# Optimization experiments

Hardware: AMD Instinct MI355X
Metric: run time of the kernel (lower is better)

Reference implementation:

```python
import jax, jax.numpy as jnp
import numpy as np

D_MODEL = 1024
NUM_HEADS = 16
D_K = D_MODEL // NUM_HEADS
CLAMP = 1e9
EPS = 1e-12


def setup_inputs() -> dict:
    key = jax.random.key(0)
    ks = jax.random.split(key, 11)
    B, S, D = 4, 2048, D_MODEL
    std = 1.0 / np.sqrt(D)
    inp = {
        'Q': jax.random.normal(ks[0], (B, S, D), jnp.float32),
        'K': jax.random.normal(ks[1], (B, S, D), jnp.float32),
        'V': jax.random.normal(ks[2], (B, S, D), jnp.float32),
        'Wq': jax.random.normal(ks[3], (D, D), jnp.float32) * std,
        'bq': jnp.zeros((D,), jnp.float32),
        'Wk': jax.random.normal(ks[4], (D, D), jnp.float32) * std,
        'bk': jnp.zeros((D,), jnp.float32),
        'Wv': jax.random.normal(ks[5], (D, D), jnp.float32) * std,
        'bv': jnp.zeros((D,), jnp.float32),
        'Wo': jax.random.normal(ks[6], (D, D), jnp.float32) * std,
        'bo': jnp.zeros((D,), jnp.float32),
    }
    return inp


def _split_heads(x):
    b, s, _ = x.shape
    return x.reshape(b, s, NUM_HEADS, D_K).transpose(0, 2, 1, 3)  # [b,h,s,dk]


def reference(Q, K, V, Wq, bq, Wk, bk, Wv, bv, Wo, bo):
    Qh = _split_heads(Q @ Wq.T + bq)
    Kh = _split_heads(K @ Wk.T + bk)
    Vh = _split_heads(V @ Wv.T + bv)
    scale = jnp.sqrt(jnp.asarray(D_K, Qh.dtype))
    scores = jnp.einsum('bhqd,bhkd->bhqk', Qh, Kh) / scale
    scores = scores - jnp.max(scores, axis=-1, keepdims=True)
    scores = jnp.clip(scores, -CLAMP, CLAMP)
    attn = jax.nn.softmax(scores, axis=-1)
    attn = jnp.clip(attn, EPS, None)
    attn = attn / jnp.sum(attn, axis=-1, keepdims=True)
    ctx = jnp.einsum('bhqk,bhkd->bhqd', attn, Vh)
    b, h, s, dk = ctx.shape
    ctx = ctx.transpose(0, 2, 1, 3).reshape(b, s, D_MODEL)
    return ctx @ Wo.T + bo
```

## Files before the change

### kernel.cpp

```cpp
#include <hip/hip_runtime.h>
#include <hip/hip_bf16.h>


typedef float  f32x4  __attribute__((ext_vector_type(4)));
typedef __bf16 bf16x8 __attribute__((ext_vector_type(8)));
typedef short  s16x8  __attribute__((ext_vector_type(8)));

#define MFMA16(a,b,c) __builtin_amdgcn_mfma_f32_16x16x32_bf16((a),(b),(c),0,0,0)

__device__ __forceinline__ unsigned short f2bf(float f) {
    union { float f; unsigned u; } v; v.f = f;
    unsigned r = v.u + 0x7fffu + ((v.u >> 16) & 1u);
    return (unsigned short)(r >> 16);
}

__device__ __forceinline__ s16x8 cvt8(const float* __restrict__ p) {
    f32x4 x = *(const f32x4*)p;
    f32x4 y = *(const f32x4*)(p + 4);
    s16x8 r;
    r[0] = (short)f2bf(x[0]); r[1] = (short)f2bf(x[1]);
    r[2] = (short)f2bf(x[2]); r[3] = (short)f2bf(x[3]);
    r[4] = (short)f2bf(y[0]); r[5] = (short)f2bf(y[1]);
    r[6] = (short)f2bf(y[2]); r[7] = (short)f2bf(y[3]);
    return r;
}

__device__ __forceinline__ void gl_lds16(const void* g, void* l) {
    __builtin_amdgcn_global_load_lds(
        (const __attribute__((address_space(1))) unsigned int*)g,
        (__attribute__((address_space(3))) unsigned int*)l, 16, 0, 0);
}

__global__ __launch_bounds__(256) void cvt_kernel(
    const float* __restrict__ src, unsigned short* __restrict__ dst, int n8)
{
    int i = blockIdx.x * 256 + threadIdx.x;
    if (i < n8) *(s16x8*)(dst + (size_t)i * 8) = cvt8(src + (size_t)i * 8);
}

template <int MODE>
__global__ __launch_bounds__(256) void gemm_bf16(
    const unsigned short* __restrict__ A,
    const unsigned short* __restrict__ W,
    const float* __restrict__ bias,
    void* __restrict__ Cv)
{
    constexpr int K = 1024;
    __shared__ unsigned short Ash[128 * 32];
    __shared__ unsigned short Bsh[128 * 32];

    const int t    = threadIdx.x;
    const int w    = t >> 6;
    const int lane = t & 63;
    const int wm   = w >> 1, wn = w & 1;
    const int lr   = lane & 15, quad = lane >> 4;

    const int m0 = blockIdx.y * 128;
    const int n0 = blockIdx.x * 128;

    const int srow = t >> 2;
    const int skp  = (t & 3) * 8;

    const unsigned short* Ap0 = A + (size_t)(m0 + srow) * K + skp;
    const unsigned short* Ap1 = Ap0 + (size_t)64 * K;
    const unsigned short* Wp0 = W + (size_t)(n0 + srow) * K + skp;
    const unsigned short* Wp1 = Wp0 + (size_t)64 * K;
    unsigned short* lA0 = &Ash[w * 512];
    unsigned short* lA1 = &Ash[2048 + w * 512];
    unsigned short* lB0 = &Bsh[w * 512];
    unsigned short* lB1 = &Bsh[2048 + w * 512];

    f32x4 acc[4][4] = {};

    for (int k0 = 0; k0 < K; k0 += 32) {
        __syncthreads();
        gl_lds16(Ap0 + k0, lA0);
        gl_lds16(Ap1 + k0, lA1);
        gl_lds16(Wp0 + k0, lB0);
        gl_lds16(Wp1 + k0, lB1);
        __syncthreads();

        bf16x8 af[4], bw[4];
#pragma unroll
        for (int i = 0; i < 4; i++)
            af[i] = *(const bf16x8*)&Ash[(wm * 64 + i * 16 + lr) * 32 + quad * 8];
#pragma unroll
        for (int j = 0; j < 4; j++)
            bw[j] = *(const bf16x8*)&Bsh[(wn * 64 + j * 16 + lr) * 32 + quad * 8];

#pragma unroll
        for (int i = 0; i < 4; i++)
#pragma unroll
            for (int j = 0; j < 4; j++)
                acc[i][j] = MFMA16(af[i], bw[j], acc[i][j]);
    }

#pragma unroll
    for (int i = 0; i < 4; i++) {
#pragma unroll
        for (int j = 0; j < 4; j++) {
            const int n = n0 + wn * 64 + j * 16 + lr;
#pragma unroll
            for (int r = 0; r < 4; r++) {
                const int m = m0 + wm * 64 + i * 16 + quad * 4 + r;
                float val = acc[i][j][r] + ((MODE == 2) ? bias[m] : bias[n]);
                if (MODE == 0) {
                    const int b = m >> 11, s = m & 2047, h = n >> 6, d = n & 63;
                    ((unsigned short*)Cv)[(((size_t)(b * 16 + h) * 2048 + s) << 6) + d] = f2bf(val);
                } else if (MODE == 1) {
                    ((float*)Cv)[(size_t)m * 1024 + n] = val;
                } else {
                    const int h = m >> 6, d = m & 63, b = n >> 11, s = n & 2047;
                    ((unsigned short*)Cv)[((size_t)(b * 16 + h) * 64 + d) * 2048 + s] = f2bf(val);
                }
            }
        }
    }
}

__global__ __launch_bounds__(256) void attn_kernel(
    const unsigned short* __restrict__ Qh,
    const unsigned short* __restrict__ Kh,
    const unsigned short* __restrict__ Vt,
    unsigned short* __restrict__ ctx)
{
    constexpr int KS = 72;
    __shared__ unsigned short Ksh[64 * KS];
    __shared__ unsigned short Vts[64 * KS];
    __shared__ unsigned short Psh[4][16 * KS];

    const int t    = threadIdx.x;
    const int w    = t >> 6;
    const int lane = t & 63;
    const int lr   = lane & 15, quad = lane >> 4;

    const int bh = blockIdx.y, qblk = blockIdx.x;
    const size_t base = (size_t)bh * 2048 * 64;
    const unsigned short* Qp = Qh + base;
    const unsigned short* Kg = Kh + base + (size_t)lane * 64 + w * 16;
    const unsigned short* Vg = Vt + base + (size_t)lane * 2048 + w * 16;

    const int q0 = qblk * 64 + w * 16;
    bf16x8 aq0 = *(const bf16x8*)(Qp + (size_t)(q0 + lr) * 64 + quad * 8);
    bf16x8 aq1 = *(const bf16x8*)(Qp + (size_t)(q0 + lr) * 64 + 32 + quad * 8);

    f32x4 Of[4] = {};
    float lsum[4] = {0.f, 0.f, 0.f, 0.f};

    for (int kb = 0; kb < 2048; kb += 64) {
        s16x8 kv0 = *(const s16x8*)(Kg + (size_t)kb * 64);
        s16x8 kv1 = *(const s16x8*)(Kg + (size_t)kb * 64 + 8);
        s16x8 vv0 = *(const s16x8*)(Vg + kb);
        s16x8 vv1 = *(const s16x8*)(Vg + kb + 8);

        __syncthreads();
        *(s16x8*)&Ksh[lane * KS + w * 16]     = kv0;
        *(s16x8*)&Ksh[lane * KS + w * 16 + 8] = kv1;
        *(s16x8*)&Vts[lane * KS + w * 16]     = vv0;
        *(s16x8*)&Vts[lane * KS + w * 16 + 8] = vv1;
        __syncthreads();

        f32x4 sc[4];
#pragma unroll
        for (int nt = 0; nt < 4; nt++) {
            const unsigned short* kr = &Ksh[(16 * nt + lr) * KS + quad * 8];
            f32x4 c = {};
            c = MFMA16(aq0, *(const bf16x8*)kr, c);
            c = MFMA16(aq1, *(const bf16x8*)(kr + 32), c);
            sc[nt] = c;
        }

#pragma unroll
        for (int r = 0; r < 4; r++) {
            float p0 = __expf(sc[0][r] * 0.125f);
            float p1 = __expf(sc[1][r] * 0.125f);
            float p2 = __expf(sc[2][r] * 0.125f);
            float p3 = __expf(sc[3][r] * 0.125f);
            lsum[r] += (p0 + p1) + (p2 + p3);
            unsigned short* pr = &Psh[w][(quad * 4 + r) * KS + lr];
            pr[0]  = f2bf(p0);
            pr[16] = f2bf(p1);
            pr[32] = f2bf(p2);
            pr[48] = f2bf(p3);
        }
        __asm__ __volatile__("s_waitcnt lgkmcnt(0)" ::: "memory");

        bf16x8 pf0 = *(const bf16x8*)&Psh[w][lr * KS + quad * 8];
        bf16x8 pf1 = *(const bf16x8*)&Psh[w][lr * KS + 32 + quad * 8];
#pragma unroll
        for (int dt = 0; dt < 4; dt++) {
            const unsigned short* vr = &Vts[(dt * 16 + lr) * KS + quad * 8];
            Of[dt] = MFMA16(pf0, *(const bf16x8*)vr, Of[dt]);
            Of[dt] = MFMA16(pf1, *(const bf16x8*)(vr + 32), Of[dt]);
        }
    }

    const int b = bh >> 4, h = bh & 15;
#pragma unroll
    for (int r = 0; r < 4; r++) {
        float l = lsum[r];
        l += __shfl_xor(l, 1);
        l += __shfl_xor(l, 2);
        l += __shfl_xor(l, 4);
        l += __shfl_xor(l, 8);
        const float inv = 1.0f / l;
        const int q = q0 + quad * 4 + r;
        unsigned short* cp = ctx + ((size_t)b * 2048 + q) * 1024 + h * 64;
#pragma unroll
        for (int dt = 0; dt < 4; dt++)
            cp[dt * 16 + lr] = f2bf(Of[dt][r] * inv);
    }
}

extern "C" void kernel_launch(void* const* d_in, const int* in_sizes, int n_in,
                              void* d_out, int out_size, void* d_ws, size_t ws_size,
                              hipStream_t stream) {
    const float* Q  = (const float*)d_in[0];
    const float* K  = (const float*)d_in[1];
    const float* V  = (const float*)d_in[2];
    const float* Wq = (const float*)d_in[3];
    const float* bq = (const float*)d_in[4];
    const float* Wk = (const float*)d_in[5];
    const float* bk = (const float*)d_in[6];
    const float* Wv = (const float*)d_in[7];
    const float* bv = (const float*)d_in[8];
    const float* Wo = (const float*)d_in[9];
    const float* bo = (const float*)d_in[10];

    const size_t EB = (size_t)8192 * 1024;
    const size_t EW = (size_t)1024 * 1024;
    unsigned short* Xb  = (unsigned short*)d_ws;
    unsigned short* Wqb = Xb  + EB;
    unsigned short* Wkb = Wqb + EW;
    unsigned short* Wvb = Wkb + EW;
    unsigned short* Wob = Wvb + EW;
    unsigned short* Qh  = Wob + EW;
    unsigned short* Kh  = Qh  + EB;
    unsigned short* Vtw = Kh  + EB;
    unsigned short* Ctx = Xb;

    const int n8b = (int)(EB / 8);
    const int n8w = (int)(EW / 8);

    cvt_kernel<<<n8w / 256, 256, 0, stream>>>(Wq, Wqb, n8w);
    cvt_kernel<<<n8w / 256, 256, 0, stream>>>(Wk, Wkb, n8w);
    cvt_kernel<<<n8w / 256, 256, 0, stream>>>(Wv, Wvb, n8w);
    cvt_kernel<<<n8w / 256, 256, 0, stream>>>(Wo, Wob, n8w);

    dim3 tb(256), gP(8, 64), gT(64, 8);

    cvt_kernel<<<n8b / 256, 256, 0, stream>>>(Q, Xb, n8b);
    gemm_bf16<0><<<gP, tb, 0, stream>>>(Xb, Wqb, bq, Qh);

    cvt_kernel<<<n8b / 256, 256, 0, stream>>>(K, Xb, n8b);
    gemm_bf16<0><<<gP, tb, 0, stream>>>(Xb, Wkb, bk, Kh);

    cvt_kernel<<<n8b / 256, 256, 0, stream>>>(V, Xb, n8b);
    gemm_bf16<2><<<gT, tb, 0, stream>>>(Wvb, Xb, bv, Vtw);

    attn_kernel<<<dim3(32, 64), tb, 0, stream>>>(Qh, Kh, Vtw, Ctx);

    gemm_bf16<1><<<gP, tb, 0, stream>>>(Ctx, Wob, bo, (float*)d_out);
}
```

Measured before the change: 424.7 us.

## Batch QKV projections into one launch, vectorize epilogues, widen attention query tiles

The three input projections now run as a single launch that picks its operands from blockIdx.z, when the workspace is large enough to hold separate bf16 copies of Q, K and V. The GEMM operands are swapped so each lane stores four contiguous outputs, which turns scalar epilogue stores into vector stores. The attention kernel gives each wave 64 query rows instead of 16, so every K/V tile staged in LDS is reused four times more, at the cost of more registers, a larger P buffer and a quarter as many blocks. Lower occupancy and fewer blocks could hurt latency hiding.

```diff
diff --git a/kernel.cpp b/kernel.cpp
--- a/kernel.cpp
+++ b/kernel.cpp
@@ -5,6 +5,7 @@
 typedef float  f32x4  __attribute__((ext_vector_type(4)));
 typedef __bf16 bf16x8 __attribute__((ext_vector_type(8)));
 typedef short  s16x8  __attribute__((ext_vector_type(8)));
+typedef short  s16x4  __attribute__((ext_vector_type(4)));
 
 #define MFMA16(a,b,c) __builtin_amdgcn_mfma_f32_16x16x32_bf16((a),(b),(c),0,0,0)
 
@@ -38,33 +39,44 @@
     if (i < n8) *(s16x8*)(dst + (size_t)i * 8) = cvt8(src + (size_t)i * 8);
 }
 
-template <int MODE>
-__global__ __launch_bounds__(256) void gemm_bf16(
-    const unsigned short* __restrict__ A,
-    const unsigned short* __restrict__ W,
-    const float* __restrict__ bias,
-    void* __restrict__ Cv)
+__global__ __launch_bounds__(256) void gemm_fused(
+    const unsigned short* __restrict__ A0, const unsigned short* __restrict__ B0,
+    const float* __restrict__ c0, void* __restrict__ d0, int m0_,
+    const unsigned short* __restrict__ A1, const unsigned short* __restrict__ B1,
+    const float* __restrict__ c1, void* __restrict__ d1, int m1_,
+    const unsigned short* __restrict__ A2, const unsigned short* __restrict__ B2,
+    const float* __restrict__ c2, void* __restrict__ d2, int m2_,
+    int zforce)
 {
+    const int z = (zforce >= 0) ? zforce : (int)blockIdx.z;
+    const unsigned short* A = (z == 0) ? A0 : (z == 1) ? A1 : A2;
+    const unsigned short* B = (z == 0) ? B0 : (z == 1) ? B1 : B2;
+    const float* bias       = (z == 0) ? c0 : (z == 1) ? c1 : c2;
+    void* dst               = (z == 0) ? d0 : (z == 1) ? d1 : d2;
+    const int mode          = (z == 0) ? m0_ : (z == 1) ? m1_ : m2_;
+
     constexpr int K = 1024;
     __shared__ unsigned short Ash[128 * 32];
     __shared__ unsigned short Bsh[128 * 32];
 
     const int t    = threadIdx.x;
     const int w    = t >> 6;
+    const int wm   = w >> 1, wn = w & 1;
     const int lane = t & 63;
-    const int wm   = w >> 1, wn = w & 1;
     const int lr   = lane & 15, quad = lane >> 4;
 
-    const int m0 = blockIdx.y * 128;
-    const int n0 = blockIdx.x * 128;
+    const int ta = (mode == 2) ? (int)blockIdx.x : (int)blockIdx.y;
+    const int tb = (mode == 2) ? (int)blockIdx.y : (int)blockIdx.x;
+    const int a0 = ta * 128;
+    const int b0 = tb * 128;
 
     const int srow = t >> 2;
     const int skp  = (t & 3) * 8;
 
-    const unsigned short* Ap0 = A + (size_t)(m0 + srow) * K + skp;
+    const unsigned short* Ap0 = A + (size_t)(a0 + srow) * K + skp;
     const unsigned short* Ap1 = Ap0 + (size_t)64 * K;
-    const unsigned short* Wp0 = W + (size_t)(n0 + srow) * K + skp;
-    const unsigned short* Wp1 = Wp0 + (size_t)64 * K;
+    const unsigned short* Bp0 = B + (size_t)(b0 + srow) * K + skp;
+    const unsigned short* Bp1 = Bp0 + (size_t)64 * K;
     unsigned short* lA0 = &Ash[w * 512];
     unsigned short* lA1 = &Ash[2048 + w * 512];
     unsigned short* lB0 = &Bsh[w * 512];
@@ -76,8 +88,8 @@
         __syncthreads();
         gl_lds16(Ap0 + k0, lA0);
         gl_lds16(Ap1 + k0, lA1);
-        gl_lds16(Wp0 + k0, lB0);
-        gl_lds16(Wp1 + k0, lB1);
+        gl_lds16(Bp0 + k0, lB0);
+        gl_lds16(Bp1 + k0, lB1);
         __syncthreads();
 
         bf16x8 af[4], bw[4];
@@ -99,20 +111,30 @@
     for (int i = 0; i < 4; i++) {
 #pragma unroll
         for (int j = 0; j < 4; j++) {
-            const int n = n0 + wn * 64 + j * 16 + lr;
-#pragma unroll
-            for (int r = 0; r < 4; r++) {
-                const int m = m0 + wm * 64 + i * 16 + quad * 4 + r;
-                float val = acc[i][j][r] + ((MODE == 2) ? bias[m] : bias[n]);
-                if (MODE == 0) {
-                    const int b = m >> 11, s = m & 2047, h = n >> 6, d = n & 63;
-                    ((unsigned short*)Cv)[(((size_t)(b * 16 + h) * 2048 + s) << 6) + d] = f2bf(val);
-                } else if (MODE == 1) {
-                    ((float*)Cv)[(size_t)m * 1024 + n] = val;
-                } else {
-                    const int h = m >> 6, d = m & 63, b = n >> 11, s = n & 2047;
-                    ((unsigned short*)Cv)[((size_t)(b * 16 + h) * 64 + d) * 2048 + s] = f2bf(val);
-                }
+            const int fa = a0 + wm * 64 + i * 16 + quad * 4;
+            const int cb = b0 + wn * 64 + j * 16 + lr;
+            if (mode == 0) {
+                f32x4 bb = *(const f32x4*)(bias + fa);
+                const int h = fa >> 6, d = fa & 63;
+                const int bb_ = cb >> 11, s = cb & 2047;
+                s16x4 pk;
+#pragma unroll
+                for (int r = 0; r < 4; r++) pk[r] = (short)f2bf(acc[i][j][r] + bb[r]);
+                *(s16x4*)((unsigned short*)dst +
+                          (((size_t)(bb_ * 16 + h) * 2048 + s) << 6) + d) = pk;
+            } else if (mode == 1) {
+                f32x4 bb = *(const f32x4*)(bias + fa);
+                f32x4 v  = acc[i][j] + bb;
+                *(f32x4*)((float*)dst + (size_t)cb * 1024 + fa) = v;
+            } else {
+                const float bb = bias[cb];
+                const int h = cb >> 6, d = cb & 63;
+                const int bb_ = fa >> 11, s = fa & 2047;
+                s16x4 pk;
+#pragma unroll
+                for (int r = 0; r < 4; r++) pk[r] = (short)f2bf(acc[i][j][r] + bb);
+                *(s16x4*)((unsigned short*)dst +
+                          ((size_t)(bb_ * 16 + h) * 64 + d) * 2048 + s) = pk;
             }
         }
     }
@@ -127,7 +149,7 @@
     constexpr int KS = 72;
     __shared__ unsigned short Ksh[64 * KS];
     __shared__ unsigned short Vts[64 * KS];
-    __shared__ unsigned short Psh[4][16 * KS];
+    __shared__ unsigned short Psh[4][64 * KS];
 
     const int t    = threadIdx.x;
     const int w    = t >> 6;
@@ -140,12 +162,18 @@
     const unsigned short* Kg = Kh + base + (size_t)lane * 64 + w * 16;
     const unsigned short* Vg = Vt + base + (size_t)lane * 2048 + w * 16;
 
-    const int q0 = qblk * 64 + w * 16;
-    bf16x8 aq0 = *(const bf16x8*)(Qp + (size_t)(q0 + lr) * 64 + quad * 8);
-    bf16x8 aq1 = *(const bf16x8*)(Qp + (size_t)(q0 + lr) * 64 + 32 + quad * 8);
-
-    f32x4 Of[4] = {};
-    float lsum[4] = {0.f, 0.f, 0.f, 0.f};
+    const int q0 = qblk * 256 + w * 64;
+
+    bf16x8 aq0[4], aq1[4];
+#pragma unroll
+    for (int s4 = 0; s4 < 4; s4++) {
+        const unsigned short* qp = Qp + (size_t)(q0 + s4 * 16 + lr) * 64 + quad * 8;
+        aq0[s4] = *(const bf16x8*)qp;
+        aq1[s4] = *(const bf16x8*)(qp + 32);
+    }
+
+    f32x4 Of[4][4] = {};
+    float lsum[4][4] = {};
 
     for (int kb = 0; kb < 2048; kb += 64) {
         s16x8 kv0 = *(const s16x8*)(Kg + (size_t)kb * 64);
@@ -160,55 +188,76 @@
         *(s16x8*)&Vts[lane * KS + w * 16 + 8] = vv1;
         __syncthreads();
 
-        f32x4 sc[4];
+        bf16x8 bk0[4], bk1[4];
 #pragma unroll
         for (int nt = 0; nt < 4; nt++) {
             const unsigned short* kr = &Ksh[(16 * nt + lr) * KS + quad * 8];
-            f32x4 c = {};
-            c = MFMA16(aq0, *(const bf16x8*)kr, c);
-            c = MFMA16(aq1, *(const bf16x8*)(kr + 32), c);
-            sc[nt] = c;
-        }
-
-#pragma unroll
-        for (int r = 0; r < 4; r++) {
-            float p0 = __expf(sc[0][r] * 0.125f);
-            float p1 = __expf(sc[1][r] * 0.125f);
-            float p2 = __expf(sc[2][r] * 0.125f);
-            float p3 = __expf(sc[3][r] * 0.125f);
-            lsum[r] += (p0 + p1) + (p2 + p3);
-            unsigned short* pr = &Psh[w][(quad * 4 + r) * KS + lr];
-            pr[0]  = f2bf(p0);
-            pr[16] = f2bf(p1);
-            pr[32] = f2bf(p2);
-            pr[48] = f2bf(p3);
+            bk0[nt] = *(const bf16x8*)kr;
+            bk1[nt] = *(const bf16x8*)(kr + 32);
+        }
+#pragma unroll
+        for (int sub = 0; sub < 4; sub++) {
+            f32x4 sc[4];
+#pragma unroll
+            for (int nt = 0; nt < 4; nt++) {
+                f32x4 c = {};
+                c = MFMA16(aq0[sub], bk0[nt], c);
+                c = MFMA16(aq1[sub], bk1[nt], c);
+                sc[nt] = c;
+            }
+#pragma unroll
+            for (int r = 0; r < 4; r++) {
+                float p0 = __expf(sc[0][r] * 0.125f);
+                float p1 = __expf(sc[1][r] * 0.125f);
+                float p2 = __expf(sc[2][r] * 0.125f);
+                float p3 = __expf(sc[3][r] * 0.125f);
+                lsum[sub][r] += (p0 + p1) + (p2 + p3);
+                unsigned short* pr = &Psh[w][(sub * 16 + quad * 4 + r) * KS + lr];
+                pr[0]  = f2bf(p0);
+                pr[16] = f2bf(p1);
+                pr[32] = f2bf(p2);
+                pr[48] = f2bf(p3);
+            }
         }
         __asm__ __volatile__("s_waitcnt lgkmcnt(0)" ::: "memory");
 
-        bf16x8 pf0 = *(const bf16x8*)&Psh[w][lr * KS + quad * 8];
-        bf16x8 pf1 = *(const bf16x8*)&Psh[w][lr * KS + 32 + quad * 8];
+        bf16x8 bv0[4], bv1[4];
 #pragma unroll
         for (int dt = 0; dt < 4; dt++) {
             const unsigned short* vr = &Vts[(dt * 16 + lr) * KS + quad * 8];
-            Of[dt] = MFMA16(pf0, *(const bf16x8*)vr, Of[dt]);
-            Of[dt] = MFMA16(pf1, *(const bf16x8*)(vr + 32), Of[dt]);
+            bv0[dt] = *(const bf16x8*)vr;
+            bv1[dt] = *(const bf16x8*)(vr + 32);
+        }
+#pragma unroll
+        for (int sub = 0; sub < 4; sub++) {
+            const unsigned short* pp = &Psh[w][(sub * 16 + lr) * KS + quad * 8];
+            bf16x8 pf0 = *(const bf16x8*)pp;
+            bf16x8 pf1 = *(const bf16x8*)(pp + 32);
+#pragma unroll
+            for (int dt = 0; dt < 4; dt++) {
+                Of[sub][dt] = MFMA16(pf0, bv0[dt], Of[sub][dt]);
+                Of[sub][dt] = MFMA16(pf1, bv1[dt], Of[sub][dt]);
+            }
         }
     }
 
     const int b = bh >> 4, h = bh & 15;
 #pragma unroll
-    for (int r = 0; r < 4; r++) {
-        float l = lsum[r];
-        l += __shfl_xor(l, 1);
-        l += __shfl_xor(l, 2);
-        l += __shfl_xor(l, 4);
-        l += __shfl_xor(l, 8);
-        const float inv = 1.0f / l;
-        const int q = q0 + quad * 4 + r;
-        unsigned short* cp = ctx + ((size_t)b * 2048 + q) * 1024 + h * 64;
-#pragma unroll
-        for (int dt = 0; dt < 4; dt++)
-            cp[dt * 16 + lr] = f2bf(Of[dt][r] * inv);
+    for (int sub = 0; sub < 4; sub++) {
+#pragma unroll
+        for (int r = 0; r < 4; r++) {
+            float l = lsum[sub][r];
+            l += __shfl_xor(l, 1);
+            l += __shfl_xor(l, 2);
+            l += __shfl_xor(l, 4);
+            l += __shfl_xor(l, 8);
+            const float inv = 1.0f / l;
+            const int q = q0 + sub * 16 + quad * 4 + r;
+            unsigned short* cp = ctx + ((size_t)b * 2048 + q) * 1024 + h * 64;
+#pragma unroll
+            for (int dt = 0; dt < 4; dt++)
+                cp[dt * 16 + lr] = f2bf(Of[sub][dt][r] * inv);
+        }
     }
 }
 
@@ -229,36 +278,76 @@
 
     const size_t EB = (size_t)8192 * 1024;
     const size_t EW = (size_t)1024 * 1024;
-    unsigned short* Xb  = (unsigned short*)d_ws;
-    unsigned short* Wqb = Xb  + EB;
-    unsigned short* Wkb = Wqb + EW;
-    unsigned short* Wvb = Wkb + EW;
-    unsigned short* Wob = Wvb + EW;
-    unsigned short* Qh  = Wob + EW;
-    unsigned short* Kh  = Qh  + EB;
-    unsigned short* Vtw = Kh  + EB;
-    unsigned short* Ctx = Xb;
-
-    const int n8b = (int)(EB / 8);
-    const int n8w = (int)(EW / 8);
-
-    cvt_kernel<<<n8w / 256, 256, 0, stream>>>(Wq, Wqb, n8w);
-    cvt_kernel<<<n8w / 256, 256, 0, stream>>>(Wk, Wkb, n8w);
-    cvt_kernel<<<n8w / 256, 256, 0, stream>>>(Wv, Wvb, n8w);
-    cvt_kernel<<<n8w / 256, 256, 0, stream>>>(Wo, Wob, n8w);
-
-    dim3 tb(256), gP(8, 64), gT(64, 8);
-
-    cvt_kernel<<<n8b / 256, 256, 0, stream>>>(Q, Xb, n8b);
-    gemm_bf16<0><<<gP, tb, 0, stream>>>(Xb, Wqb, bq, Qh);
-
-    cvt_kernel<<<n8b / 256, 256, 0, stream>>>(K, Xb, n8b);
-    gemm_bf16<0><<<gP, tb, 0, stream>>>(Xb, Wkb, bk, Kh);
-
-    cvt_kernel<<<n8b / 256, 256, 0, stream>>>(V, Xb, n8b);
-    gemm_bf16<2><<<gT, tb, 0, stream>>>(Wvb, Xb, bv, Vtw);
-
-    attn_kernel<<<dim3(32, 64), tb, 0, stream>>>(Qh, Kh, Vtw, Ctx);
-
-    gemm_bf16<1><<<gP, tb, 0, stream>>>(Ctx, Wob, bo, (float*)d_out);
-}
+    const int n8b = (int)(EB / 8), n8w = (int)(EW / 8);
+    dim3 tb(256);
+
+    const bool fused = ws_size >= (6 * EB + 4 * EW) * 2;
+
+    if (fused) {
+        unsigned short* Xq  = (unsigned short*)d_ws;
+        unsigned short* Xk  = Xq + EB;
+        unsigned short* Xv  = Xk + EB;
+        unsigned short* Wqb = Xv + EB;
+        unsigned short* Wkb = Wqb + EW;
+        unsigned short* Wvb = Wkb + EW;
+        unsigned short* Wob = Wvb + EW;
+        unsigned short* Qh  = Wob + EW;
+        unsigned short* Kh  = Qh + EB;
+        unsigned short* Vtw = Kh + EB;
+        unsigned short* Ctx = Xq;
+
+        cvt_kernel<<<n8w / 256, tb, 0, stream>>>(Wq, Wqb, n8w);
+        cvt_kernel<<<n8w / 256, tb, 0, stream>>>(Wk, Wkb, n8w);
+        cvt_kernel<<<n8w / 256, tb, 0, stream>>>(Wv, Wvb, n8w);
+        cvt_kernel<<<n8w / 256, tb, 0, stream>>>(Wo, Wob, n8w);
+        cvt_kernel<<<n8b / 256, tb, 0, stream>>>(Q, Xq, n8b);
+        cvt_kernel<<<n8b / 256, tb, 0, stream>>>(K, Xk, n8b);
+        cvt_kernel<<<n8b / 256, tb, 0, stream>>>(V, Xv, n8b);
+
+        gemm_fused<<<dim3(64, 8, 3), tb, 0, stream>>>(
+            Wqb, Xq, bq, Qh, 0,
+            Wkb, Xk, bk, Kh, 0,
+            Xv, Wvb, bv, Vtw, 2,
+            -1);
+
+        attn_kernel<<<dim3(8, 64), tb, 0, stream>>>(Qh, Kh, Vtw, Ctx);
+
+        gemm_fused<<<dim3(64, 8, 1), tb, 0, stream>>>(
+            Wob, Ctx, bo, d_out, 1,
+            Wob, Ctx, bo, d_out, 1,
+            Wob, Ctx, bo, d_out, 1,
+            0);
+    } else {
+        unsigned short* Xb  = (unsigned short*)d_ws;
+        unsigned short* Wqb = Xb + EB;
+        unsigned short* Wkb = Wqb + EW;
+        unsigned short* Wvb = Wkb + EW;
+        unsigned short* Wob = Wvb + EW;
+        unsigned short* Qh  = Wob + EW;
+        unsigned short* Kh  = Qh + EB;
+        unsigned short* Vtw = Kh + EB;
+        unsigned short* Ctx = Xb;
+
+        cvt_kernel<<<n8w / 256, tb, 0, stream>>>(Wq, Wqb, n8w);
+        cvt_kernel<<<n8w / 256, tb, 0, stream>>>(Wk, Wkb, n8w);
+        cvt_kernel<<<n8w / 256, tb, 0, stream>>>(Wv, Wvb, n8w);
+        cvt_kernel<<<n8w / 256, tb, 0, stream>>>(Wo, Wob, n8w);
+
+        cvt_kernel<<<n8b / 256, tb, 0, stream>>>(Q, Xb, n8b);
+        gemm_fused<<<dim3(64, 8, 1), tb, 0, stream>>>(
+            Wqb, Xb, bq, Qh, 0,  Wqb, Xb, bq, Qh, 0,  Wqb, Xb, bq, Qh, 0, 0);
+
+        cvt_kernel<<<n8b / 256, tb, 0, stream>>>(K, Xb, n8b);
+        gemm_fused<<<dim3(64, 8, 1), tb, 0, stream>>>(
+            Wkb, Xb, bk, Kh, 0,  Wkb, Xb, bk, Kh, 0,  Wkb, Xb, bk, Kh, 0, 0);
+
+        cvt_kernel<<<n8b / 256, tb, 0, stream>>>(V, Xb, n8b);
+        gemm_fused<<<dim3(64, 8, 1), tb, 0, stream>>>(
+            Xb, Wvb, bv, Vtw, 2,  Xb, Wvb, bv, Vtw, 2,  Xb, Wvb, bv, Vtw, 2, 0);
+
+        attn_kernel<<<dim3(8, 64), tb, 0, stream>>>(Qh, Kh, Vtw, Ctx);
+
+        gemm_fused<<<dim3(64, 8, 1), tb, 0, stream>>>(
+            Wob, Ctx, bo, d_out, 1,  Wob, Ctx, bo, d_out, 1,  Wob, Ctx, bo, d_out, 1, 0);
+    }
+}
```

Result: slower. 468.5 us (+10.3%).
